# Kernel optimization log

Hardware: AMD Instinct MI355X
Metric: run time of the kernel (lower is better)

## Reference

```python
import jax, jax.numpy as jnp
import numpy as np
import math

B, S, L, K, NSTEPS = 32, 128, 4096, 129, 10
PAD = K // 2  # torch: int(kernel.shape[-1]/2)


def _grouped_xcorr(x, w):
    # torch F.conv1d semantics (cross-correlation), groups = channels
    # x: [B,C,L] f32, w: [C,1,K] f32 -> [B,C,L]
    return jax.lax.conv_general_dilated(
        x, w, window_strides=(1,), padding=[(PAD, PAD)],
        dimension_numbers=('NCH', 'OIH', 'NCH'), feature_group_count=x.shape[1])


def _matched_filter(x_re, x_im, k_re, k_im):
    # complex grouped conv with conj(kernel) repeated per pulse
    wc_re = jnp.tile(k_re[None, None, :], (S, 1, 1))
    wc_im = jnp.tile(-k_im[None, None, :], (S, 1, 1))  # conj
    out_re = _grouped_xcorr(x_re, wc_re) - _grouped_xcorr(x_im, wc_im)
    out_im = _grouped_xcorr(x_re, wc_im) + _grouped_xcorr(x_im, wc_re)
    return out_re + 1j * out_im  # complex64 [B,S,L]


def _produce_rd(x, w_mag, w_phase):
    phase = jnp.arctan(w_phase)                    # [B,S]
    norm_mag = S * jax.nn.softmax(w_mag, axis=-1)  # [B,S]
    iq = (norm_mag * jnp.exp(-1j * phase))[..., None] * x
    return jnp.fft.fftshift(jnp.fft.fft(iq, axis=-2), axes=-2)


def _circular_weighted_mean(w):
    # circular weighted mean of index over last axis; returns (magnitude, index)
    N = w.shape[-1]
    ang = (2.0 * jnp.pi / N) * jnp.arange(N, dtype=w.dtype)
    z = jnp.sum(w * jnp.exp(1j * ang), axis=-1)
    return jnp.abs(z), jnp.angle(z) / (2.0 * jnp.pi) * N


def _snr(rd):
    Bn, nfft, Ln = rd.shape
    e = jnp.abs(rd) ** 2                                   # [B,S,L]
    flat_idx = jnp.argmax(e.reshape(Bn, -1), axis=1)
    max_range = flat_idx % Ln                              # [B] (indices: constant wrt grad)
    col = jnp.take_along_axis(e, max_range[:, None, None], axis=2)[..., 0]  # [B,S]
    _, peak_idx = _circular_weighted_mean(col)
    # torch rounds + casts to int -> detached index
    idx = jax.lax.stop_gradient(jnp.round(peak_idx)).astype(jnp.int32) % nfft
    peak = jnp.take_along_axis(col, idx[:, None], axis=1)[:, 0]
    noise = (jnp.sum(col, axis=-1) - peak) / (nfft - 1)
    return 10.0 * jnp.log10(peak) - 10.0 * jnp.log10(noise)


def setup_inputs() -> dict:
    key = jax.random.key(0)
    ks = jax.random.split(key, 5)
    return {
        'x_re': jax.random.normal(ks[0], (B, S, L), jnp.float32),
        'x_im': jax.random.normal(ks[1], (B, S, L), jnp.float32),
        'kernel_re': jax.random.normal(ks[2], (K,), jnp.float32),
        'kernel_im': jax.random.normal(ks[3], (K,), jnp.float32),
        'log_step_mag': -2.0 * jnp.ones((S, NSTEPS), jnp.float32),
        'log_step_phase': -2.0 * jnp.ones((S, NSTEPS), jnp.float32),
        'w_phase_init': jax.random.uniform(ks[4], (B, S), jnp.float32),
    }


def reference(x_re, x_im, kernel_re, kernel_im, log_step_mag, log_step_phase, w_phase_init):
    x = _matched_filter(x_re, x_im, kernel_re, kernel_im)  # [B,S,L] complex64
    w_mag = jnp.ones((B, S), jnp.float32)
    w_phase = w_phase_init

    def loss_sum(wm, wp):
        return jnp.sum(_snr(_produce_rd(x, wm, wp)))

    grad_fn = jax.grad(loss_sum, argnums=(0, 1))
    ln10 = math.log(10.0)
    for i in range(NSTEPS):
        # torch detaches w_mag/w_phase before the inner autograd.grad
        g_mag, g_phase = grad_fn(jax.lax.stop_gradient(w_mag),
                                 jax.lax.stop_gradient(w_phase))
        lr_mag = jnp.exp(log_step_mag[:, i] * ln10)    # 10**log_step
        lr_phase = jnp.exp(log_step_phase[:, i] * ln10)
        w_mag = w_mag + lr_mag * g_mag
        w_phase = w_phase + lr_phase * g_phase
    return jnp.mean(_snr(_produce_rd(x, w_mag, w_phase)))
```

## Files before the change

kernel.cpp:

```cpp
#include <hip/hip_runtime.h>

#define BB 32
#define SS 128
#define LL 4096
#define KK 129
#define NST 10

constexpr double PI_D = 3.141592653589793238462643383279502884;
constexpr double red_sin(double x){
  double x2 = x*x, t = x, r = x;
  t *= -x2/6.0;   r += t;
  t *= -x2/20.0;  r += t;
  t *= -x2/42.0;  r += t;
  t *= -x2/72.0;  r += t;
  t *= -x2/110.0; r += t;
  t *= -x2/156.0; r += t;
  t *= -x2/210.0; r += t;
  t *= -x2/272.0; r += t;
  return r;
}
constexpr double csin_d(double x){
  while (x >  PI_D) x -= 2.0*PI_D;
  while (x < -PI_D) x += 2.0*PI_D;
  if (x >  PI_D*0.5)      x =  PI_D - x;
  else if (x < -PI_D*0.5) x = -PI_D - x;
  return red_sin(x);
}
constexpr double ccos_d(double x){ return csin_d(x + PI_D*0.5); }
struct TWT { float c[64]; float s[64]; };
constexpr TWT make_tw(){
  TWT t{};
  for (int j = 0; j < 64; j++){
    double a = -2.0*PI_D*(double)j/128.0;
    t.c[j] = (float)ccos_d(a);
    t.s[j] = (float)csin_d(a);
  }
  return t;
}
constexpr TWT TW = make_tw();

#define PHYS8(i) ((i) + ((i) >> 3))

__global__ __launch_bounds__(256) void mf_kernel(const float* __restrict__ xr,
                                                 const float* __restrict__ xi,
                                                 const float* __restrict__ kr,
                                                 const float* __restrict__ ki,
                                                 float2* __restrict__ out)
{
  const int row = blockIdx.x >> 1;
  const int l0  = (blockIdx.x & 1) * 2048;
  const int t   = threadIdx.x;
  __shared__ float2 xs[2456];
  __shared__ float2 ks[132];
  if (t < KK) ks[t] = make_float2(kr[t], ki[t]);

  const float* xrr = xr + (size_t)row*LL;
  const float* xir = xi + (size_t)row*LL;
  for (int i4 = t; i4 < 544; i4 += 256){
    const int g0 = l0 - 64 + i4*4;
    float4 a, c;
    if (g0 >= 0 && g0 + 3 < LL){
      a = *(const float4*)(xrr + g0);
      c = *(const float4*)(xir + g0);
    } else {
      float av[4], cv[4];
      #pragma unroll
      for (int e = 0; e < 4; ++e){
        const int g = g0 + e;
        const bool ok = (g >= 0 && g < LL);
        av[e] = ok ? xrr[g] : 0.0f;
        cv[e] = ok ? xir[g] : 0.0f;
      }
      a = make_float4(av[0],av[1],av[2],av[3]);
      c = make_float4(cv[0],cv[1],cv[2],cv[3]);
    }
    const int i = i4*4;
    const int p = PHYS8(i);
    xs[p]   = make_float2(a.x, c.x);
    xs[p+1] = make_float2(a.y, c.y);
    xs[p+2] = make_float2(a.z, c.z);
    xs[p+3] = make_float2(a.w, c.w);
  }
  __syncthreads();

  const int base_l = t*8;
  float wr_[16], wi_[16];
  #pragma unroll
  for (int v = 0; v < 12; v += 2){
    const float4 p = *(const float4*)(&xs[PHYS8(base_l + v)]);
    wr_[v]   = p.x; wi_[v]   = p.y;
    wr_[v+1] = p.z; wi_[v+1] = p.w;
  }

  float2 acc[8];
  #pragma unroll
  for (int j = 0; j < 8; j++) acc[j] = make_float2(0.0f, 0.0f);

  #pragma unroll 1
  for (int q8 = 0; q8 < 8; ++q8){
    #pragma unroll
    for (int qq = 0; qq < 4; ++qq){
      const int q = q8*4 + qq;
      float4 p0, p1;
      const bool doref = (q < 31);
      if (doref){
        const int v0 = base_l + q*4 + 12;
        p0 = *(const float4*)(&xs[PHYS8(v0)]);
        p1 = *(const float4*)(&xs[PHYS8(v0 + 2)]);
      }
      float2 wv[4];
      #pragma unroll
      for (int kk = 0; kk < 4; ++kk) wv[kk] = ks[q*4 + kk];
      #pragma unroll
      for (int kk = 0; kk < 4; ++kk){
        const float wx = wv[kk].x, wy = wv[kk].y;
        #pragma unroll
        for (int j = 0; j < 8; ++j){
          const int sl = (qq*4 + kk + j) & 15;
          const float xvr = wr_[sl], xvi = wi_[sl];
          acc[j].x = fmaf(xvr, wx, acc[j].x);
          acc[j].x = fmaf(xvi, wy, acc[j].x);
          acc[j].y = fmaf(xvi, wx, acc[j].y);
          acc[j].y = fmaf(-xvr, wy, acc[j].y);
        }
      }
      if (doref){
        const int s0 = (qq*4 + 12) & 15;
        wr_[s0]   = p0.x; wi_[s0]   = p0.y;
        wr_[s0+1] = p0.z; wi_[s0+1] = p0.w;
        wr_[s0+2] = p1.x; wi_[s0+2] = p1.y;
        wr_[s0+3] = p1.z; wi_[s0+3] = p1.w;
      }
    }
  }
  {
    const float2 w = ks[128];
    #pragma unroll
    for (int j = 0; j < 8; ++j){
      const float xvr = wr_[j], xvi = wi_[j];
      acc[j].x = fmaf(xvr, w.x, acc[j].x);
      acc[j].x = fmaf(xvi, w.y, acc[j].x);
      acc[j].y = fmaf(xvi, w.x, acc[j].y);
      acc[j].y = fmaf(-xvr, w.y, acc[j].y);
    }
  }

  float4* orow = (float4*)(out + (size_t)row*LL + l0 + base_l);
  #pragma unroll
  for (int q = 0; q < 4; ++q){
    orow[q] = make_float4(acc[2*q].x, acc[2*q].y, acc[2*q+1].x, acc[2*q+1].y);
  }
}

__global__ __launch_bounds__(512) void tr_kernel(const float2* __restrict__ xmf,
                                                 float4* __restrict__ xt2)
{
  const int b = blockIdx.y;
  const int l0 = blockIdx.x * 64;
  const int tid = threadIdx.x;
  __shared__ float ldr[SS][65];
  __shared__ float ldi[SS][65];
  #pragma unroll
  for (int it = 0; it < 8; ++it){
    const int flat = it*512 + tid;
    const int s  = flat >> 5;
    const int c4 = flat & 31;
    const float4 p = *(const float4*)(xmf + ((size_t)(b*SS + s))*LL + l0 + 2*c4);
    const int sw = 8*(s >> 5);
    ldr[s][(2*c4   + sw) & 63] = p.x;  ldi[s][(2*c4   + sw) & 63] = p.y;
    ldr[s][(2*c4+1 + sw) & 63] = p.z;  ldi[s][(2*c4+1 + sw) & 63] = p.w;
  }
  __syncthreads();
  float4* dst = xt2 + ((size_t)(b*256 + blockIdx.x*4) * 16) * 64;
  #pragma unroll
  for (int it = 0; it < 8; ++it){
    const int flat = it*512 + tid;
    const int lane = flat & 63;
    const int i   = (flat >> 6) & 15;
    const int lgl = flat >> 10;
    const int fl = lane >> 2, r = lane & 3;
    const int lrow = lgl*16 + fl;
    const int s0 = r*32 + 2*i;
    const int col = (lrow + 8*r) & 63;
    dst[flat] = make_float4(ldr[s0][col], ldi[s0][col], ldr[s0+1][col], ldi[s0+1][col]);
  }
}

__global__ void init_kernel(const float* __restrict__ wpi,
                            float* __restrict__ w_mag, float* __restrict__ w_phase,
                            float2* __restrict__ cvec, unsigned long long* __restrict__ slots,
                            float* __restrict__ out)
{
  const int i = blockIdx.x*256 + threadIdx.x;
  if (i < BB*SS){
    float wp = wpi[i];
    w_mag[i] = 1.0f;
    w_phase[i] = wp;
    float phi = atanf(wp);
    float s, c;
    sincosf(phi, &s, &c);
    cvec[i] = make_float2(c, -s);
  }
  if (i < BB) slots[i] = 0ull;
  if (i == 0) out[0] = 0.0f;
}

template<int SPAN, int N>
__device__ __forceinline__ void fstage(float2* v){
  #pragma unroll
  for (int b0 = 0; b0 < N; b0 += 2*SPAN){
    #pragma unroll
    for (int j = 0; j < SPAN; j++){
      const int i0 = b0 + j, i1 = b0 + j + SPAN;
      float ax = v[i0].x, ay = v[i0].y, bx = v[i1].x, by = v[i1].y;
      float sx = ax - bx, sy = ay - by;
      v[i0].x = ax + bx; v[i0].y = ay + by;
      const int tj = j * (64 / SPAN);
      if (tj == 0){
        v[i1].x = sx; v[i1].y = sy;
      } else if (tj == 32){
        v[i1].x = sy; v[i1].y = -sx;
      } else {
        const float wr = TW.c[tj], wi = TW.s[tj];
        v[i1].x = sx*wr - sy*wi;
        v[i1].y = sy*wr + sx*wi;
      }
    }
  }
}

__device__ __forceinline__ void scan_fft_tail(float2* v, int r, int tid, int l,
                                              unsigned long long* wred, int nwave,
                                              unsigned long long* slot)
{
  {
    const bool hi = (r & 2) != 0;
    const float sgn = hi ? -1.0f : 1.0f;
    const bool odd = (r & 1) != 0;
    #pragma unroll
    for (int j = 0; j < 32; ++j){
      float px = __shfl_xor(v[j].x, 2);
      float py = __shfl_xor(v[j].y, 2);
      float ux = fmaf(sgn, v[j].x, px);
      float uy = fmaf(sgn, v[j].y, py);
      float wr = hi ? (odd ? TW.s[j] : TW.c[j]) : 1.0f;
      float wi = hi ? (odd ? -TW.c[j] : TW.s[j]) : 0.0f;
      v[j].x = ux*wr - uy*wi;
      v[j].y = uy*wr + ux*wi;
    }
  }
  {
    const bool hi = (r & 1) != 0;
    const float sgn = hi ? -1.0f : 1.0f;
    #pragma unroll
    for (int j = 0; j < 32; ++j){
      float px = __shfl_xor(v[j].x, 1);
      float py = __shfl_xor(v[j].y, 1);
      float ux = fmaf(sgn, v[j].x, px);
      float uy = fmaf(sgn, v[j].y, py);
      float wr = hi ? TW.c[2*j] : 1.0f;
      float wi = hi ? TW.s[2*j] : 0.0f;
      v[j].x = ux*wr - uy*wi;
      v[j].y = uy*wr + ux*wi;
    }
  }
  fstage<16,32>(v); fstage<8,32>(v); fstage<4,32>(v); fstage<2,32>(v); fstage<1,32>(v);

  float mm = 0.0f;
  #pragma unroll
  for (int j = 0; j < 32; ++j) mm = fmaxf(mm, v[j].x*v[j].x + v[j].y*v[j].y);
  mm = fmaxf(mm, __shfl_xor(mm, 1));
  mm = fmaxf(mm, __shfl_xor(mm, 2));

  unsigned long long pk = ((unsigned long long)__float_as_uint(mm) << 32) | (unsigned int)l;
  #pragma unroll
  for (int m = 4; m < 64; m <<= 1){
    unsigned long long o = __shfl_xor(pk, m);
    if (o > pk) pk = o;
  }
  if ((tid & 63) == 0) wred[tid >> 6] = pk;
  __syncthreads();
  if (tid == 0){
    unsigned long long best = wred[0];
    for (int w = 1; w < nwave; ++w) if (wred[w] > best) best = wred[w];
    atomicMax(slot, best);
  }
}

__global__ __launch_bounds__(256) void scan_t_kernel(const float4* __restrict__ xt2,
                                                     const float2* __restrict__ cvec,
                                                     unsigned long long* __restrict__ slots)
{
  const int b = blockIdx.y;
  const int tid = threadIdx.x;
  const int f = tid >> 2, r = tid & 3;
  const int l = blockIdx.x*64 + f;
  const int w = tid >> 6;
  const int lg = blockIdx.x*4 + w;
  __shared__ float2 csh[SS];
  __shared__ unsigned long long wred[4];
  if (tid < SS) csh[tid] = cvec[b*SS + tid];
  __syncthreads();

  const float4* base = xt2 + ((size_t)(b*(LL/16) + lg) * 16) * 64 + (tid & 63);
  float2 v[32];
  #pragma unroll
  for (int i = 0; i < 16; ++i){
    const float4 p = base[i*64];
    v[2*i]   = make_float2(p.x, p.y);
    v[2*i+1] = make_float2(p.z, p.w);
  }
  #pragma unroll
  for (int j = 0; j < 32; ++j){
    const float2 c = csh[r*32 + j];
    const float2 x = v[j];
    v[j].x = c.x*x.x - c.y*x.y;
    v[j].y = c.x*x.y + c.y*x.x;
  }
  scan_fft_tail(v, r, tid, l, wred, 4, slots + b);
}

__global__ __launch_bounds__(512, 4) void scan_o_kernel(const float2* __restrict__ xmf,
                                                        const float2* __restrict__ cvec,
                                                        unsigned long long* __restrict__ slots)
{
  const int b = blockIdx.y;
  const int tid = threadIdx.x;
  const int l0 = blockIdx.x * 128;
  __shared__ float2 csh[SS];
  __shared__ float2 xsh[64][130];
  __shared__ unsigned long long wred[8];
  if (tid < SS) csh[tid] = cvec[b*SS + tid];

  const int f = tid >> 2, r = tid & 3;
  float2 v[32];

  #pragma unroll 1
  for (int h = 0; h < 2; ++h){
    __syncthreads();
    const float2* src = xmf + ((size_t)(b*SS + h*64))*LL + l0;
    #pragma unroll
    for (int it = 0; it < 8; ++it){
      const int flat = it*512 + tid;
      const int s1 = flat >> 6;
      const int c4 = flat & 63;
      const float4 vv = *(const float4*)(src + (size_t)s1*LL + c4*2);
      *(float4*)(&xsh[s1][c4*2]) = vv;
    }
    __syncthreads();
    if ((r >> 1) == h){
      #pragma unroll
      for (int j = 0; j < 32; ++j){
        const int rowi = (r & 1)*32 + j;
        const float2 x = xsh[rowi][f];
        const float2 c = csh[r*32 + j];
        v[j].x = c.x*x.x - c.y*x.y;
        v[j].y = c.x*x.y + c.y*x.x;
      }
    }
  }
  scan_fft_tail(v, r, tid, l0 + f, wred, 8, slots + b);
}

__device__ __forceinline__ float wredsum(float v){
  #pragma unroll
  for (int m = 1; m < 64; m <<= 1) v += __shfl_xor(v, m);
  return v;
}
__device__ __forceinline__ float wredmax(float v){
  #pragma unroll
  for (int m = 1; m < 64; m <<= 1) v = fmaxf(v, __shfl_xor(v, m));
  return v;
}
__device__ __forceinline__ float bsum256(float v, float* red4, int t){
  v = wredsum(v);
  __syncthreads();
  if ((t & 63) == 0) red4[t >> 6] = v;
  __syncthreads();
  return red4[0] + red4[1] + red4[2] + red4[3];
}
__device__ __forceinline__ float bmax256(float v, float* red4, int t){
  v = wredmax(v);
  __syncthreads();
  if ((t & 63) == 0) red4[t >> 6] = v;
  __syncthreads();
  return fmaxf(fmaxf(red4[0], red4[1]), fmaxf(red4[2], red4[3]));
}

__global__ __launch_bounds__(256) void step_kernel(const float2* __restrict__ xmf,
                                                   float* __restrict__ w_mag,
                                                   float* __restrict__ w_phase,
                                                   float2* __restrict__ cvec,
                                                   unsigned long long* __restrict__ slots,
                                                   const float* __restrict__ lsm,
                                                   const float* __restrict__ lsp,
                                                   int stepi, int isFinal,
                                                   float* __restrict__ out)
{
  const int b = blockIdx.x, t = threadIdx.x;
  const int s = t >> 1, h = t & 1;
  __shared__ float2 ysh[SS];
  __shared__ float twc[SS], tws[SS];
  __shared__ float red4[4];
  __shared__ float speak;
  __shared__ int sidx;

  const int rbin = (int)(slots[b] & 0xffffffffull);
  const float wm0 = w_mag[b*SS + s];
  const float wp0 = w_phase[b*SS + s];
  const float2 xc = xmf[((size_t)(b*SS + s))*LL + rbin];
  float phi = atanf(wp0);
  float sph, cph;
  sincosf(phi, &sph, &cph);
  {
    int id = t & 127;
    float sv, cv;
    sincosf((float)(2.0*PI_D/128.0) * (float)id, &sv, &cv);
    twc[id] = cv; tws[id] = -sv;
  }
  float mx = bmax256(wm0, red4, t);
  float ex = expf(wm0 - mx);
  float sm = bsum256(ex, red4, t) * 0.5f;
  float m = 128.0f * ex / sm;
  float cre = m*cph, cim = -m*sph;
  ysh[s] = make_float2(cre*xc.x - cim*xc.y, cre*xc.y + cim*xc.x);
  __syncthreads();

  const int k = s;
  float Fr = 0.0f, Fi = 0.0f;
  #pragma unroll 8
  for (int q = 0; q < 64; ++q){
    int s2 = h*64 + q;
    int id = (k*s2) & 127;
    float wr = twc[id], wi = tws[id];
    float2 ys = ysh[s2];
    Fr += wr*ys.x - wi*ys.y;
    Fi += wr*ys.y + wi*ys.x;
  }
  Fr += __shfl_xor(Fr, 1);
  Fi += __shfl_xor(Fi, 1);
  const int u = (k + 64) & 127;
  float colu = Fr*Fr + Fi*Fi;

  float total = bsum256(colu, red4, t) * 0.5f;
  float zre = bsum256(colu * twc[u], red4, t) * 0.5f;
  float zim = bsum256(colu * (-tws[u]), red4, t) * 0.5f;
  if (t == 0){
    float ang = atan2f(zim, zre);
    float pidx = ang * (128.0f/(2.0f*(float)PI_D));
    sidx = ((int)rintf(pidx)) & 127;
  }
  __syncthreads();
  const int idx = sidx;
  if (u == idx && h == 0) speak = colu;
  __syncthreads();
  const float peak = speak;
  const float noise = (total - peak) * (1.0f/127.0f);

  if (isFinal){
    if (t == 0) atomicAdd(out, 10.0f*(log10f(peak) - log10f(noise)) * (1.0f/(float)BB));
    return;
  }

  constexpr float C10 = 4.342944819032518f;
  float g = (u == idx) ? (C10/peak) : (-C10/(127.0f*noise));
  __syncthreads();
  ysh[k] = make_float2(2.0f*g*Fr, 2.0f*g*Fi);
  __syncthreads();

  float Tr = 0.0f, Ti = 0.0f;
  #pragma unroll 8
  for (int q = 0; q < 64; ++q){
    int kk = h*64 + q;
    int id = (s*kk) & 127;
    float wr = twc[id], wi = -tws[id];
    float2 G = ysh[kk];
    Tr += wr*G.x - wi*G.y;
    Ti += wr*G.y + wi*G.x;
  }
  Tr += __shfl_xor(Tr, 1);
  Ti += __shfl_xor(Ti, 1);

  float Hr = xc.x*Tr + xc.y*Ti;
  float Hi = xc.x*Ti - xc.y*Tr;
  float dm   = Hr*cph - Hi*sph;
  float dphi = -m*(Hr*sph + Hi*cph);
  float S1 = bsum256(m*dm, red4, t) * 0.5f;
  float gwm = m*(dm - S1*(1.0f/128.0f));
  float gwp = dphi / (1.0f + wp0*wp0);

  constexpr float LN10 = 2.302585092994046f;
  float lrm = expf(lsm[s*NST + stepi] * LN10);
  float lrp = expf(lsp[s*NST + stepi] * LN10);
  float wm1 = wm0 + lrm*gwm;
  float wp1 = wp0 + lrp*gwp;
  if (h == 0){
    w_mag[b*SS + s] = wm1;
    w_phase[b*SS + s] = wp1;
  }

  float mx2 = bmax256(wm1, red4, t);
  float ex2 = expf(wm1 - mx2);
  float sm2 = bsum256(ex2, red4, t) * 0.5f;
  float m2 = 128.0f * ex2 / sm2;
  float phi2 = atanf(wp1);
  float s2v, c2v;
  sincosf(phi2, &s2v, &c2v);
  if (h == 0) cvec[b*SS + s] = make_float2(m2*c2v, -m2*s2v);
  if (t == 0) slots[b] = 0ull;
}

extern "C" void kernel_launch(void* const* d_in, const int* in_sizes, int n_in,
                              void* d_out, int out_size, void* d_ws, size_t ws_size,
                              hipStream_t stream)
{
  const float* x_re = (const float*)d_in[0];
  const float* x_im = (const float*)d_in[1];
  const float* k_re = (const float*)d_in[2];
  const float* k_im = (const float*)d_in[3];
  const float* lsm  = (const float*)d_in[4];
  const float* lsp  = (const float*)d_in[5];
  const float* wpi  = (const float*)d_in[6];
  float* out = (float*)d_out;

  char* ws = (char*)d_ws;
  size_t off = 0;
  float2* xmf = (float2*)(ws + off);                 off += (size_t)BB*SS*LL*sizeof(float2);
  unsigned long long* slots = (unsigned long long*)(ws + off); off += 256;
  float* w_mag   = (float*)(ws + off);               off += (size_t)BB*SS*4;
  float* w_phase = (float*)(ws + off);               off += (size_t)BB*SS*4;
  float2* cvec   = (float2*)(ws + off);              off += (size_t)BB*SS*8;
  const size_t off_base = off;
  float4* xt2 = (float4*)(ws + off);                 off += (size_t)BB*SS*LL*sizeof(float2);
  const int useT = (ws_size >= off) ? 1 : 0;
  if (ws_size < off_base) return;

  mf_kernel<<<BB*SS*2, 256, 0, stream>>>(x_re, x_im, k_re, k_im, xmf);
  init_kernel<<<(BB*SS + 255)/256, 256, 0, stream>>>(wpi, w_mag, w_phase, cvec, slots, out);
  if (useT) tr_kernel<<<dim3(LL/64, BB), 512, 0, stream>>>(xmf, xt2);

  for (int i = 0; i < NST; i++){
    if (useT) scan_t_kernel<<<dim3(LL/64, BB), 256, 0, stream>>>(xt2, cvec, slots);
    else      scan_o_kernel<<<dim3(LL/128, BB), 512, 0, stream>>>(xmf, cvec, slots);
    step_kernel<<<BB, 256, 0, stream>>>(xmf, w_mag, w_phase, cvec, slots, lsm, lsp, i, 0, out);
  }
  if (useT) scan_t_kernel<<<dim3(LL/64, BB), 256, 0, stream>>>(xt2, cvec, slots);
  else      scan_o_kernel<<<dim3(LL/128, BB), 512, 0, stream>>>(xmf, cvec, slots);
  step_kernel<<<BB, 256, 0, stream>>>(xmf, w_mag, w_phase, cvec, slots, lsm, lsp, 0, 1, out);
}
```

Measured before the change: 795.9 us.

## Fuse per-batch step into scan kernel via last-block counter; split matched-filter smem into planar arrays

Each scan block increments a per-batch atomic counter after its argmax, and the last block for each batch runs the weight-update step body in place. This removes the separate step_kernel launch and its launch gap for each of the 11 iterations. The matched-filter kernel also stores real and imaginary parts in separate shared arrays, so each refill reads them with float4 loads. The cost is threadfences and atomics at the end of every scan block, plus a serialized step tail running on a single block per batch.

```diff
diff --git a/kernel.cpp b/kernel.cpp
--- a/kernel.cpp
+++ b/kernel.cpp
@@ -50,7 +50,8 @@
   const int row = blockIdx.x >> 1;
   const int l0  = (blockIdx.x & 1) * 2048;
   const int t   = threadIdx.x;
-  __shared__ float2 xs[2456];
+  __shared__ float xsr[2448];
+  __shared__ float xsi[2448];
   __shared__ float2 ks[132];
   if (t < KK) ks[t] = make_float2(kr[t], ki[t]);
 
@@ -74,22 +75,20 @@
       a = make_float4(av[0],av[1],av[2],av[3]);
       c = make_float4(cv[0],cv[1],cv[2],cv[3]);
     }
-    const int i = i4*4;
-    const int p = PHYS8(i);
-    xs[p]   = make_float2(a.x, c.x);
-    xs[p+1] = make_float2(a.y, c.y);
-    xs[p+2] = make_float2(a.z, c.z);
-    xs[p+3] = make_float2(a.w, c.w);
+    const int p = PHYS8(i4*4);
+    *(float4*)&xsr[p] = a;
+    *(float4*)&xsi[p] = c;
   }
   __syncthreads();
 
   const int base_l = t*8;
   float wr_[16], wi_[16];
   #pragma unroll
-  for (int v = 0; v < 12; v += 2){
-    const float4 p = *(const float4*)(&xs[PHYS8(base_l + v)]);
-    wr_[v]   = p.x; wi_[v]   = p.y;
-    wr_[v+1] = p.z; wi_[v+1] = p.w;
+  for (int v = 0; v < 12; v += 4){
+    const float4 pr = *(const float4*)(&xsr[PHYS8(base_l + v)]);
+    const float4 pi = *(const float4*)(&xsi[PHYS8(base_l + v)]);
+    wr_[v]=pr.x; wr_[v+1]=pr.y; wr_[v+2]=pr.z; wr_[v+3]=pr.w;
+    wi_[v]=pi.x; wi_[v+1]=pi.y; wi_[v+2]=pi.z; wi_[v+3]=pi.w;
   }
 
   float2 acc[8];
@@ -101,12 +100,12 @@
     #pragma unroll
     for (int qq = 0; qq < 4; ++qq){
       const int q = q8*4 + qq;
-      float4 p0, p1;
+      float4 pr, pi;
       const bool doref = (q < 31);
       if (doref){
         const int v0 = base_l + q*4 + 12;
-        p0 = *(const float4*)(&xs[PHYS8(v0)]);
-        p1 = *(const float4*)(&xs[PHYS8(v0 + 2)]);
+        pr = *(const float4*)(&xsr[PHYS8(v0)]);
+        pi = *(const float4*)(&xsi[PHYS8(v0)]);
       }
       float2 wv[4];
       #pragma unroll
@@ -126,10 +125,8 @@
       }
       if (doref){
         const int s0 = (qq*4 + 12) & 15;
-        wr_[s0]   = p0.x; wi_[s0]   = p0.y;
-        wr_[s0+1] = p0.z; wi_[s0+1] = p0.w;
-        wr_[s0+2] = p1.x; wi_[s0+2] = p1.y;
-        wr_[s0+3] = p1.z; wi_[s0+3] = p1.w;
+        wr_[s0]=pr.x; wr_[s0+1]=pr.y; wr_[s0+2]=pr.z; wr_[s0+3]=pr.w;
+        wi_[s0]=pi.x; wi_[s0+1]=pi.y; wi_[s0+2]=pi.z; wi_[s0+3]=pi.w;
       }
     }
   }
@@ -189,7 +186,7 @@
 __global__ void init_kernel(const float* __restrict__ wpi,
                             float* __restrict__ w_mag, float* __restrict__ w_phase,
                             float2* __restrict__ cvec, unsigned long long* __restrict__ slots,
-                            float* __restrict__ out)
+                            unsigned int* __restrict__ cnt, float* __restrict__ out)
 {
   const int i = blockIdx.x*256 + threadIdx.x;
   if (i < BB*SS){
@@ -201,7 +198,7 @@
     sincosf(phi, &s, &c);
     cvec[i] = make_float2(c, -s);
   }
-  if (i < BB) slots[i] = 0ull;
+  if (i < BB){ slots[i] = 0ull; cnt[i] = 0u; }
   if (i == 0) out[0] = 0.0f;
 }
 
@@ -287,9 +284,160 @@
   }
 }
 
-__global__ __launch_bounds__(256) void scan_t_kernel(const float4* __restrict__ xt2,
-                                                     const float2* __restrict__ cvec,
-                                                     unsigned long long* __restrict__ slots)
+__device__ __forceinline__ float wredsum(float v){
+  #pragma unroll
+  for (int m = 1; m < 64; m <<= 1) v += __shfl_xor(v, m);
+  return v;
+}
+__device__ __forceinline__ float wredmax(float v){
+  #pragma unroll
+  for (int m = 1; m < 64; m <<= 1) v = fmaxf(v, __shfl_xor(v, m));
+  return v;
+}
+__device__ __forceinline__ float bsum256(float v, float* red4, int t){
+  v = wredsum(v);
+  __syncthreads();
+  if ((t & 63) == 0) red4[t >> 6] = v;
+  __syncthreads();
+  return red4[0] + red4[1] + red4[2] + red4[3];
+}
+__device__ __forceinline__ float bmax256(float v, float* red4, int t){
+  v = wredmax(v);
+  __syncthreads();
+  if ((t & 63) == 0) red4[t >> 6] = v;
+  __syncthreads();
+  return fmaxf(fmaxf(red4[0], red4[1]), fmaxf(red4[2], red4[3]));
+}
+
+__device__ __forceinline__ void step_body(int b, int t,
+                                          const float2* __restrict__ xmf,
+                                          float* __restrict__ w_mag,
+                                          float* __restrict__ w_phase,
+                                          float2* __restrict__ cvec,
+                                          unsigned long long* __restrict__ slots,
+                                          const float* __restrict__ lsm,
+                                          const float* __restrict__ lsp,
+                                          int stepi, int isFinal,
+                                          float* __restrict__ out,
+                                          int rbin,
+                                          float2* ysh, float* twc, float* tws,
+                                          float* red4, float* speakp, int* sidxp)
+{
+  const int s = t >> 1, h = t & 1;
+  const float wm0 = w_mag[b*SS + s];
+  const float wp0 = w_phase[b*SS + s];
+  const float2 xc = xmf[((size_t)(b*SS + s))*LL + rbin];
+  float phi = atanf(wp0);
+  float sph, cph;
+  sincosf(phi, &sph, &cph);
+  {
+    int id = t & 127;
+    float sv, cv;
+    sincosf((float)(2.0*PI_D/128.0) * (float)id, &sv, &cv);
+    twc[id] = cv; tws[id] = -sv;
+  }
+  float mx = bmax256(wm0, red4, t);
+  float ex = expf(wm0 - mx);
+  float sm = bsum256(ex, red4, t) * 0.5f;
+  float m = 128.0f * ex / sm;
+  float cre = m*cph, cim = -m*sph;
+  ysh[s] = make_float2(cre*xc.x - cim*xc.y, cre*xc.y + cim*xc.x);
+  __syncthreads();
+
+  const int k = s;
+  float Fr = 0.0f, Fi = 0.0f;
+  #pragma unroll 8
+  for (int q = 0; q < 64; ++q){
+    int s2 = h*64 + q;
+    int id = (k*s2) & 127;
+    float wr = twc[id], wi = tws[id];
+    float2 ys = ysh[s2];
+    Fr += wr*ys.x - wi*ys.y;
+    Fi += wr*ys.y + wi*ys.x;
+  }
+  Fr += __shfl_xor(Fr, 1);
+  Fi += __shfl_xor(Fi, 1);
+  const int u = (k + 64) & 127;
+  float colu = Fr*Fr + Fi*Fi;
+
+  float total = bsum256(colu, red4, t) * 0.5f;
+  float zre = bsum256(colu * twc[u], red4, t) * 0.5f;
+  float zim = bsum256(colu * (-tws[u]), red4, t) * 0.5f;
+  if (t == 0){
+    float ang = atan2f(zim, zre);
+    float pidx = ang * (128.0f/(2.0f*(float)PI_D));
+    *sidxp = ((int)rintf(pidx)) & 127;
+  }
+  __syncthreads();
+  const int idx = *sidxp;
+  if (u == idx && h == 0) *speakp = colu;
+  __syncthreads();
+  const float peak = *speakp;
+  const float noise = (total - peak) * (1.0f/127.0f);
+
+  if (isFinal){
+    if (t == 0) atomicAdd(out, 10.0f*(log10f(peak) - log10f(noise)) * (1.0f/(float)BB));
+    return;
+  }
+
+  constexpr float C10 = 4.342944819032518f;
+  float g = (u == idx) ? (C10/peak) : (-C10/(127.0f*noise));
+  __syncthreads();
+  ysh[k] = make_float2(2.0f*g*Fr, 2.0f*g*Fi);
+  __syncthreads();
+
+  float Tr = 0.0f, Ti = 0.0f;
+  #pragma unroll 8
+  for (int q = 0; q < 64; ++q){
+    int kk = h*64 + q;
+    int id = (s*kk) & 127;
+    float wr = twc[id], wi = -tws[id];
+    float2 G = ysh[kk];
+    Tr += wr*G.x - wi*G.y;
+    Ti += wr*G.y + wi*G.x;
+  }
+  Tr += __shfl_xor(Tr, 1);
+  Ti += __shfl_xor(Ti, 1);
+
+  float Hr = xc.x*Tr + xc.y*Ti;
+  float Hi = xc.x*Ti - xc.y*Tr;
+  float dm   = Hr*cph - Hi*sph;
+  float dphi = -m*(Hr*sph + Hi*cph);
+  float S1 = bsum256(m*dm, red4, t) * 0.5f;
+  float gwm = m*(dm - S1*(1.0f/128.0f));
+  float gwp = dphi / (1.0f + wp0*wp0);
+
+  constexpr float LN10 = 2.302585092994046f;
+  float lrm = expf(lsm[s*NST + stepi] * LN10);
+  float lrp = expf(lsp[s*NST + stepi] * LN10);
+  float wm1 = wm0 + lrm*gwm;
+  float wp1 = wp0 + lrp*gwp;
+  if (h == 0){
+    w_mag[b*SS + s] = wm1;
+    w_phase[b*SS + s] = wp1;
+  }
+
+  float mx2 = bmax256(wm1, red4, t);
+  float ex2 = expf(wm1 - mx2);
+  float sm2 = bsum256(ex2, red4, t) * 0.5f;
+  float m2 = 128.0f * ex2 / sm2;
+  float phi2 = atanf(wp1);
+  float s2v, c2v;
+  sincosf(phi2, &s2v, &c2v);
+  if (h == 0) cvec[b*SS + s] = make_float2(m2*c2v, -m2*s2v);
+}
+
+__global__ __launch_bounds__(256) void scan_step_kernel(const float4* __restrict__ xt2,
+                                                        const float2* __restrict__ xmf,
+                                                        float* __restrict__ w_mag,
+                                                        float* __restrict__ w_phase,
+                                                        float2* __restrict__ cvec,
+                                                        unsigned long long* __restrict__ slots,
+                                                        unsigned int* __restrict__ cnt,
+                                                        const float* __restrict__ lsm,
+                                                        const float* __restrict__ lsp,
+                                                        int stepi, int isFinal,
+                                                        float* __restrict__ out)
 {
   const int b = blockIdx.y;
   const int tid = threadIdx.x;
@@ -299,6 +447,13 @@
   const int lg = blockIdx.x*4 + w;
   __shared__ float2 csh[SS];
   __shared__ unsigned long long wred[4];
+  __shared__ int lastFlag;
+  __shared__ float2 ysh[SS];
+  __shared__ float twc[SS], tws[SS];
+  __shared__ float red4[4];
+  __shared__ float speak;
+  __shared__ int sidx;
+
   if (tid < SS) csh[tid] = cvec[b*SS + tid];
   __syncthreads();
 
@@ -318,6 +473,26 @@
     v[j].y = c.x*x.y + c.y*x.x;
   }
   scan_fft_tail(v, r, tid, l, wred, 4, slots + b);
+
+  __threadfence();
+  if (tid == 0){
+    unsigned int prev = atomicAdd(&cnt[b], 1u);
+    lastFlag = (prev == (LL/64) - 1);
+  }
+  __syncthreads();
+  if (!lastFlag) return;
+  __threadfence();
+
+  const unsigned long long sl = atomicAdd(slots + b, 0ull);
+  const int rbin = (int)(sl & 0xffffffffull);
+
+  step_body(b, tid, xmf, w_mag, w_phase, cvec, slots, lsm, lsp, stepi, isFinal, out,
+            rbin, ysh, twc, tws, red4, &speak, &sidx);
+
+  if (tid == 0){
+    atomicExch(slots + b, 0ull);
+    atomicExch(&cnt[b], 0u);
+  }
 }
 
 __global__ __launch_bounds__(512, 4) void scan_o_kernel(const float2* __restrict__ xmf,
@@ -362,31 +537,6 @@
   scan_fft_tail(v, r, tid, l0 + f, wred, 8, slots + b);
 }
 
-__device__ __forceinline__ float wredsum(float v){
-  #pragma unroll
-  for (int m = 1; m < 64; m <<= 1) v += __shfl_xor(v, m);
-  return v;
-}
-__device__ __forceinline__ float wredmax(float v){
-  #pragma unroll
-  for (int m = 1; m < 64; m <<= 1) v = fmaxf(v, __shfl_xor(v, m));
-  return v;
-}
-__device__ __forceinline__ float bsum256(float v, float* red4, int t){
-  v = wredsum(v);
-  __syncthreads();
-  if ((t & 63) == 0) red4[t >> 6] = v;
-  __syncthreads();
-  return red4[0] + red4[1] + red4[2] + red4[3];
-}
-__device__ __forceinline__ float bmax256(float v, float* red4, int t){
-  v = wredmax(v);
-  __syncthreads();
-  if ((t & 63) == 0) red4[t >> 6] = v;
-  __syncthreads();
-  return fmaxf(fmaxf(red4[0], red4[1]), fmaxf(red4[2], red4[3]));
-}
-
 __global__ __launch_bounds__(256) void step_kernel(const float2* __restrict__ xmf,
                                                    float* __restrict__ w_mag,
                                                    float* __restrict__ w_phase,
@@ -398,115 +548,14 @@
                                                    float* __restrict__ out)
 {
   const int b = blockIdx.x, t = threadIdx.x;
-  const int s = t >> 1, h = t & 1;
   __shared__ float2 ysh[SS];
   __shared__ float twc[SS], tws[SS];
   __shared__ float red4[4];
   __shared__ float speak;
   __shared__ int sidx;
-
   const int rbin = (int)(slots[b] & 0xffffffffull);
-  const float wm0 = w_mag[b*SS + s];
-  const float wp0 = w_phase[b*SS + s];
-  const float2 xc = xmf[((size_t)(b*SS + s))*LL + rbin];
-  float phi = atanf(wp0);
-  float sph, cph;
-  sincosf(phi, &sph, &cph);
-  {
-    int id = t & 127;
-    float sv, cv;
-    sincosf((float)(2.0*PI_D/128.0) * (float)id, &sv, &cv);
-    twc[id] = cv; tws[id] = -sv;
-  }
-  float mx = bmax256(wm0, red4, t);
-  float ex = expf(wm0 - mx);
-  float sm = bsum256(ex, red4, t) * 0.5f;
-  float m = 128.0f * ex / sm;
-  float cre = m*cph, cim = -m*sph;
-  ysh[s] = make_float2(cre*xc.x - cim*xc.y, cre*xc.y + cim*xc.x);
-  __syncthreads();
-
-  const int k = s;
-  float Fr = 0.0f, Fi = 0.0f;
-  #pragma unroll 8
-  for (int q = 0; q < 64; ++q){
-    int s2 = h*64 + q;
-    int id = (k*s2) & 127;
-    float wr = twc[id], wi = tws[id];
-    float2 ys = ysh[s2];
-    Fr += wr*ys.x - wi*ys.y;
-    Fi += wr*ys.y + wi*ys.x;
-  }
-  Fr += __shfl_xor(Fr, 1);
-  Fi += __shfl_xor(Fi, 1);
-  const int u = (k + 64) & 127;
-  float colu = Fr*Fr + Fi*Fi;
-
-  float total = bsum256(colu, red4, t) * 0.5f;
-  float zre = bsum256(colu * twc[u], red4, t) * 0.5f;
-  float zim = bsum256(colu * (-tws[u]), red4, t) * 0.5f;
-  if (t == 0){
-    float ang = atan2f(zim, zre);
-    float pidx = ang * (128.0f/(2.0f*(float)PI_D));
-    sidx = ((int)rintf(pidx)) & 127;
-  }
-  __syncthreads();
-  const int idx = sidx;
-  if (u == idx && h == 0) speak = colu;
-  __syncthreads();
-  const float peak = speak;
-  const float noise = (total - peak) * (1.0f/127.0f);
-
-  if (isFinal){
-    if (t == 0) atomicAdd(out, 10.0f*(log10f(peak) - log10f(noise)) * (1.0f/(float)BB));
-    return;
-  }
-
-  constexpr float C10 = 4.342944819032518f;
-  float g = (u == idx) ? (C10/peak) : (-C10/(127.0f*noise));
-  __syncthreads();
-  ysh[k] = make_float2(2.0f*g*Fr, 2.0f*g*Fi);
-  __syncthreads();
-
-  float Tr = 0.0f, Ti = 0.0f;
-  #pragma unroll 8
-  for (int q = 0; q < 64; ++q){
-    int kk = h*64 + q;
-    int id = (s*kk) & 127;
-    float wr = twc[id], wi = -tws[id];
-    float2 G = ysh[kk];
-    Tr += wr*G.x - wi*G.y;
-    Ti += wr*G.y + wi*G.x;
-  }
-  Tr += __shfl_xor(Tr, 1);
-  Ti += __shfl_xor(Ti, 1);
-
-  float Hr = xc.x*Tr + xc.y*Ti;
-  float Hi = xc.x*Ti - xc.y*Tr;
-  float dm   = Hr*cph - Hi*sph;
-  float dphi = -m*(Hr*sph + Hi*cph);
-  float S1 = bsum256(m*dm, red4, t) * 0.5f;
-  float gwm = m*(dm - S1*(1.0f/128.0f));
-  float gwp = dphi / (1.0f + wp0*wp0);
-
-  constexpr float LN10 = 2.302585092994046f;
-  float lrm = expf(lsm[s*NST + stepi] * LN10);
-  float lrp = expf(lsp[s*NST + stepi] * LN10);
-  float wm1 = wm0 + lrm*gwm;
-  float wp1 = wp0 + lrp*gwp;
-  if (h == 0){
-    w_mag[b*SS + s] = wm1;
-    w_phase[b*SS + s] = wp1;
-  }
-
-  float mx2 = bmax256(wm1, red4, t);
-  float ex2 = expf(wm1 - mx2);
-  float sm2 = bsum256(ex2, red4, t) * 0.5f;
-  float m2 = 128.0f * ex2 / sm2;
-  float phi2 = atanf(wp1);
-  float s2v, c2v;
-  sincosf(phi2, &s2v, &c2v);
-  if (h == 0) cvec[b*SS + s] = make_float2(m2*c2v, -m2*s2v);
+  step_body(b, t, xmf, w_mag, w_phase, cvec, slots, lsm, lsp, stepi, isFinal, out,
+            rbin, ysh, twc, tws, red4, &speak, &sidx);
   if (t == 0) slots[b] = 0ull;
 }
 
@@ -527,6 +576,7 @@
   size_t off = 0;
   float2* xmf = (float2*)(ws + off);                 off += (size_t)BB*SS*LL*sizeof(float2);
   unsigned long long* slots = (unsigned long long*)(ws + off); off += 256;
+  unsigned int* cnt = (unsigned int*)(ws + off);     off += 256;
   float* w_mag   = (float*)(ws + off);               off += (size_t)BB*SS*4;
   float* w_phase = (float*)(ws + off);               off += (size_t)BB*SS*4;
   float2* cvec   = (float2*)(ws + off);              off += (size_t)BB*SS*8;
@@ -536,15 +586,21 @@
   if (ws_size < off_base) return;
 
   mf_kernel<<<BB*SS*2, 256, 0, stream>>>(x_re, x_im, k_re, k_im, xmf);
-  init_kernel<<<(BB*SS + 255)/256, 256, 0, stream>>>(wpi, w_mag, w_phase, cvec, slots, out);
-  if (useT) tr_kernel<<<dim3(LL/64, BB), 512, 0, stream>>>(xmf, xt2);
-
-  for (int i = 0; i < NST; i++){
-    if (useT) scan_t_kernel<<<dim3(LL/64, BB), 256, 0, stream>>>(xt2, cvec, slots);
-    else      scan_o_kernel<<<dim3(LL/128, BB), 512, 0, stream>>>(xmf, cvec, slots);
-    step_kernel<<<BB, 256, 0, stream>>>(xmf, w_mag, w_phase, cvec, slots, lsm, lsp, i, 0, out);
-  }
-  if (useT) scan_t_kernel<<<dim3(LL/64, BB), 256, 0, stream>>>(xt2, cvec, slots);
-  else      scan_o_kernel<<<dim3(LL/128, BB), 512, 0, stream>>>(xmf, cvec, slots);
-  step_kernel<<<BB, 256, 0, stream>>>(xmf, w_mag, w_phase, cvec, slots, lsm, lsp, 0, 1, out);
-}
+  init_kernel<<<(BB*SS + 255)/256, 256, 0, stream>>>(wpi, w_mag, w_phase, cvec, slots, cnt, out);
+
+  if (useT){
+    tr_kernel<<<dim3(LL/64, BB), 512, 0, stream>>>(xmf, xt2);
+    for (int i = 0; i < NST; i++)
+      scan_step_kernel<<<dim3(LL/64, BB), 256, 0, stream>>>(xt2, xmf, w_mag, w_phase, cvec,
+                                                            slots, cnt, lsm, lsp, i, 0, out);
+    scan_step_kernel<<<dim3(LL/64, BB), 256, 0, stream>>>(xt2, xmf, w_mag, w_phase, cvec,
+                                                          slots, cnt, lsm, lsp, 0, 1, out);
+  } else {
+    for (int i = 0; i < NST; i++){
+      scan_o_kernel<<<dim3(LL/128, BB), 512, 0, stream>>>(xmf, cvec, slots);
+      step_kernel<<<BB, 256, 0, stream>>>(xmf, w_mag, w_phase, cvec, slots, lsm, lsp, i, 0, out);
+    }
+    scan_o_kernel<<<dim3(LL/128, BB), 512, 0, stream>>>(xmf, cvec, slots);
+    step_kernel<<<BB, 256, 0, stream>>>(xmf, w_mag, w_phase, cvec, slots, lsm, lsp, 0, 1, out);
+  }
+}
```

New measurement: 805.6 us. About the same (+1.2%).

## Fuse transpose into first scan pass and read filter taps from global

Applied to the files above, without the earlier changes.

Merges the standalone transpose kernel with the first scan iteration. The transposed tile already sits in LDS, so the first scan computes from it directly while still writing xt2 for later iterations. This saves one full read of the transposed buffer and one launch. The matched-filter kernel also drops its LDS copy of the 129 filter taps and reads them straight from global memory as uniform scalar loads, trading LDS traffic for scalar loads inside the hot loop.

```diff
diff --git a/kernel.cpp b/kernel.cpp
--- a/kernel.cpp
+++ b/kernel.cpp
@@ -51,8 +51,6 @@
   const int l0  = (blockIdx.x & 1) * 2048;
   const int t   = threadIdx.x;
   __shared__ float2 xs[2456];
-  __shared__ float2 ks[132];
-  if (t < KK) ks[t] = make_float2(kr[t], ki[t]);
 
   const float* xrr = xr + (size_t)row*LL;
   const float* xir = xi + (size_t)row*LL;
@@ -108,12 +106,10 @@
         p0 = *(const float4*)(&xs[PHYS8(v0)]);
         p1 = *(const float4*)(&xs[PHYS8(v0 + 2)]);
       }
-      float2 wv[4];
-      #pragma unroll
-      for (int kk = 0; kk < 4; ++kk) wv[kk] = ks[q*4 + kk];
       #pragma unroll
       for (int kk = 0; kk < 4; ++kk){
-        const float wx = wv[kk].x, wy = wv[kk].y;
+        const float wx = kr[q*4 + kk];
+        const float wy = ki[q*4 + kk];
         #pragma unroll
         for (int j = 0; j < 8; ++j){
           const int sl = (qq*4 + kk + j) & 15;
@@ -134,14 +130,14 @@
     }
   }
   {
-    const float2 w = ks[128];
+    const float wx = kr[128], wy = ki[128];
     #pragma unroll
     for (int j = 0; j < 8; ++j){
       const float xvr = wr_[j], xvi = wi_[j];
-      acc[j].x = fmaf(xvr, w.x, acc[j].x);
-      acc[j].x = fmaf(xvi, w.y, acc[j].x);
-      acc[j].y = fmaf(xvi, w.x, acc[j].y);
-      acc[j].y = fmaf(-xvr, w.y, acc[j].y);
+      acc[j].x = fmaf(xvr, wx, acc[j].x);
+      acc[j].x = fmaf(xvi, wy, acc[j].x);
+      acc[j].y = fmaf(xvi, wx, acc[j].y);
+      acc[j].y = fmaf(-xvr, wy, acc[j].y);
     }
   }
 
@@ -149,40 +145,6 @@
   #pragma unroll
   for (int q = 0; q < 4; ++q){
     orow[q] = make_float4(acc[2*q].x, acc[2*q].y, acc[2*q+1].x, acc[2*q+1].y);
-  }
-}
-
-__global__ __launch_bounds__(512) void tr_kernel(const float2* __restrict__ xmf,
-                                                 float4* __restrict__ xt2)
-{
-  const int b = blockIdx.y;
-  const int l0 = blockIdx.x * 64;
-  const int tid = threadIdx.x;
-  __shared__ float ldr[SS][65];
-  __shared__ float ldi[SS][65];
-  #pragma unroll
-  for (int it = 0; it < 8; ++it){
-    const int flat = it*512 + tid;
-    const int s  = flat >> 5;
-    const int c4 = flat & 31;
-    const float4 p = *(const float4*)(xmf + ((size_t)(b*SS + s))*LL + l0 + 2*c4);
-    const int sw = 8*(s >> 5);
-    ldr[s][(2*c4   + sw) & 63] = p.x;  ldi[s][(2*c4   + sw) & 63] = p.y;
-    ldr[s][(2*c4+1 + sw) & 63] = p.z;  ldi[s][(2*c4+1 + sw) & 63] = p.w;
-  }
-  __syncthreads();
-  float4* dst = xt2 + ((size_t)(b*256 + blockIdx.x*4) * 16) * 64;
-  #pragma unroll
-  for (int it = 0; it < 8; ++it){
-    const int flat = it*512 + tid;
-    const int lane = flat & 63;
-    const int i   = (flat >> 6) & 15;
-    const int lgl = flat >> 10;
-    const int fl = lane >> 2, r = lane & 3;
-    const int lrow = lgl*16 + fl;
-    const int s0 = r*32 + 2*i;
-    const int col = (lrow + 8*r) & 63;
-    dst[flat] = make_float4(ldr[s0][col], ldi[s0][col], ldr[s0+1][col], ldi[s0+1][col]);
   }
 }
 
@@ -287,6 +249,61 @@
   }
 }
 
+__global__ __launch_bounds__(256) void tr_scan_kernel(const float2* __restrict__ xmf,
+                                                      float4* __restrict__ xt2,
+                                                      const float2* __restrict__ cvec,
+                                                      unsigned long long* __restrict__ slots)
+{
+  const int b = blockIdx.y;
+  const int l0 = blockIdx.x * 64;
+  const int tid = threadIdx.x;
+  __shared__ float ldr[SS][65];
+  __shared__ float ldi[SS][65];
+  __shared__ float2 csh[SS];
+  __shared__ unsigned long long wred[4];
+  if (tid < SS) csh[tid] = cvec[b*SS + tid];
+
+  #pragma unroll
+  for (int it = 0; it < 16; ++it){
+    const int flat = it*256 + tid;
+    const int s  = flat >> 5;
+    const int c4 = flat & 31;
+    const float4 p = *(const float4*)(xmf + ((size_t)(b*SS + s))*LL + l0 + 2*c4);
+    const int sw = 8*(s >> 5);
+    ldr[s][(2*c4   + sw) & 63] = p.x;  ldi[s][(2*c4   + sw) & 63] = p.y;
+    ldr[s][(2*c4+1 + sw) & 63] = p.z;  ldi[s][(2*c4+1 + sw) & 63] = p.w;
+  }
+  __syncthreads();
+
+  float4* dst = xt2 + ((size_t)(b*256 + blockIdx.x*4) * 16) * 64;
+  #pragma unroll
+  for (int it = 0; it < 16; ++it){
+    const int flat = it*256 + tid;
+    const int lane = flat & 63;
+    const int i   = (flat >> 6) & 15;
+    const int lgl = flat >> 10;
+    const int fl = lane >> 2, rr = lane & 3;
+    const int lrow = lgl*16 + fl;
+    const int s0 = rr*32 + 2*i;
+    const int col = (lrow + 8*rr) & 63;
+    dst[flat] = make_float4(ldr[s0][col], ldi[s0][col], ldr[s0+1][col], ldi[s0+1][col]);
+  }
+
+  const int f = tid >> 2, r = tid & 3;
+  const int l = l0 + f;
+  float2 v[32];
+  #pragma unroll
+  for (int j = 0; j < 32; ++j){
+    const int rowi = r*32 + j;
+    const int col = (f + 8*r) & 63;
+    const float2 x = make_float2(ldr[rowi][col], ldi[rowi][col]);
+    const float2 c = csh[rowi];
+    v[j].x = c.x*x.x - c.y*x.y;
+    v[j].y = c.x*x.y + c.y*x.x;
+  }
+  scan_fft_tail(v, r, tid, l, wred, 4, slots + b);
+}
+
 __global__ __launch_bounds__(256) void scan_t_kernel(const float4* __restrict__ xt2,
                                                      const float2* __restrict__ cvec,
                                                      unsigned long long* __restrict__ slots)
@@ -537,14 +554,22 @@
 
   mf_kernel<<<BB*SS*2, 256, 0, stream>>>(x_re, x_im, k_re, k_im, xmf);
   init_kernel<<<(BB*SS + 255)/256, 256, 0, stream>>>(wpi, w_mag, w_phase, cvec, slots, out);
-  if (useT) tr_kernel<<<dim3(LL/64, BB), 512, 0, stream>>>(xmf, xt2);
-
-  for (int i = 0; i < NST; i++){
-    if (useT) scan_t_kernel<<<dim3(LL/64, BB), 256, 0, stream>>>(xt2, cvec, slots);
-    else      scan_o_kernel<<<dim3(LL/128, BB), 512, 0, stream>>>(xmf, cvec, slots);
-    step_kernel<<<BB, 256, 0, stream>>>(xmf, w_mag, w_phase, cvec, slots, lsm, lsp, i, 0, out);
-  }
-  if (useT) scan_t_kernel<<<dim3(LL/64, BB), 256, 0, stream>>>(xt2, cvec, slots);
-  else      scan_o_kernel<<<dim3(LL/128, BB), 512, 0, stream>>>(xmf, cvec, slots);
-  step_kernel<<<BB, 256, 0, stream>>>(xmf, w_mag, w_phase, cvec, slots, lsm, lsp, 0, 1, out);
-}
+
+  if (useT){
+    tr_scan_kernel<<<dim3(LL/64, BB), 256, 0, stream>>>(xmf, xt2, cvec, slots);
+    step_kernel<<<BB, 256, 0, stream>>>(xmf, w_mag, w_phase, cvec, slots, lsm, lsp, 0, 0, out);
+    for (int i = 1; i < NST; i++){
+      scan_t_kernel<<<dim3(LL/64, BB), 256, 0, stream>>>(xt2, cvec, slots);
+      step_kernel<<<BB, 256, 0, stream>>>(xmf, w_mag, w_phase, cvec, slots, lsm, lsp, i, 0, out);
+    }
+    scan_t_kernel<<<dim3(LL/64, BB), 256, 0, stream>>>(xt2, cvec, slots);
+    step_kernel<<<BB, 256, 0, stream>>>(xmf, w_mag, w_phase, cvec, slots, lsm, lsp, 0, 1, out);
+  } else {
+    for (int i = 0; i < NST; i++){
+      scan_o_kernel<<<dim3(LL/128, BB), 512, 0, stream>>>(xmf, cvec, slots);
+      step_kernel<<<BB, 256, 0, stream>>>(xmf, w_mag, w_phase, cvec, slots, lsm, lsp, i, 0, out);
+    }
+    scan_o_kernel<<<dim3(LL/128, BB), 512, 0, stream>>>(xmf, cvec, slots);
+    step_kernel<<<BB, 256, 0, stream>>>(xmf, w_mag, w_phase, cvec, slots, lsm, lsp, 0, 1, out);
+  }
+}
```

Measured after the change: 768.9 us. 1.04x faster.
